# Performance work log

Measured on AMD Instinct MI355X. Metric: run time of the kernel, lower is better.

The kernel has to match this reference:

```python
import jax, jax.numpy as jnp
import numpy as np
from jax import lax

H = 145; W = 145; BANDS = 200; D_MODEL = 128; NUM_CLASSES = 17
# Mamba2 defaults: expand=2, headdim=64, d_state=128, d_conv=4, ngroups=1
D_INNER = 256; NHEADS = 4; HEADDIM = 64; D_STATE = 128; D_CONV = 4
D_IN_PROJ = 2 * D_INNER + 2 * D_STATE + NHEADS  # 772
CONV_DIM = D_INNER + 2 * D_STATE                # 512


def _gelu(x):
    return jax.nn.gelu(x, approximate=False)


def _ln(x, g, b, eps=1e-5):
    m = jnp.mean(x, -1, keepdims=True)
    v = jnp.mean((x - m) ** 2, -1, keepdims=True)
    return (x - m) * lax.rsqrt(v + eps) * g + b


def _adaptive_pool_last(x, out):
    # PyTorch AdaptiveAvgPool semantics along the last axis via integral image
    L = x.shape[-1]
    i = np.arange(out)
    starts = (i * L) // out
    ends = -((-(i + 1) * L) // out)  # ceil((i+1)*L/out)
    cs = jnp.concatenate([jnp.zeros(x.shape[:-1] + (1,), x.dtype), jnp.cumsum(x, -1)], -1)
    return (cs[..., ends] - cs[..., starts]) / jnp.asarray(ends - starts, x.dtype)


def _mamba2(u, in_w, conv_w, conv_b, dt_bias, A_log, D, norm_w, out_w):
    # u: (L, D_MODEL). Faithful Mamba2 reference path (batch=1 squeezed).
    L = u.shape[0]
    zxbcdt = u @ in_w                      # (L, 772)
    z = zxbcdt[:, :D_INNER]                # (L, 256)
    xBC = zxbcdt[:, D_INNER:2 * D_INNER + 2 * D_STATE]  # (L, 512)
    dt = jax.nn.softplus(zxbcdt[:, -NHEADS:] + dt_bias)  # (L, 4)
    # causal depthwise conv1d, kernel D_CONV, then SiLU
    xp = jnp.pad(xBC, ((D_CONV - 1, 0), (0, 0)))
    xBC = sum(xp[k:k + L] * conv_w[:, k] for k in range(D_CONV)) + conv_b
    xBC = jax.nn.silu(xBC)
    xh = xBC[:, :D_INNER].reshape(L, NHEADS, HEADDIM)     # (L, h, p)
    Bm = xBC[:, D_INNER:D_INNER + D_STATE]                # (L, n)
    Cm = xBC[:, D_INNER + D_STATE:]                       # (L, n)
    A = -jnp.exp(A_log)                                   # (h,)

    def step(state, inp):
        dt_t, x_t, B_t, C_t = inp          # (h,), (h,p), (n,), (n,)
        dA = jnp.exp(dt_t * A)             # (h,)
        state = state * dA[:, None, None] + (dt_t[:, None] * x_t)[:, :, None] * B_t[None, None, :]
        y_t = jnp.einsum('hpn,n->hp', state, C_t)
        return state, y_t

    s0 = jnp.zeros((NHEADS, HEADDIM, D_STATE), u.dtype)
    _, y = lax.scan(step, s0, (dt, xh, Bm, Cm))           # y: (L, h, p)
    y = y + D[None, :, None] * xh
    y = y.reshape(L, D_INNER) * jax.nn.silu(z)            # gated
    y = y * lax.rsqrt(jnp.mean(y * y, -1, keepdims=True) + 1e-5) * norm_w  # RMSNormGated
    return y @ out_w                                      # (L, D_MODEL)


def _forward(x, ln_pre_g, ln_pre_b, fe_w1, fe_b1, fe_w2, fe_b2,
             cv_w1, cv_b1, cv_w2, cv_b2, mp_w, mp_b, mp_ln_g, mp_ln_b,
             m_in_w, m_conv_w, m_conv_b, m_dt_bias, m_A_log, m_D, m_norm_w, m_out_w,
             cls_ln_g, cls_ln_b, cls_w1, cls_b1, cls_w2, cls_b2, cls_w3, cls_b3):
    h, w, _ = x.shape
    xn = _ln(x, ln_pre_g, ln_pre_b)
    # MLP feature branch
    f = _gelu(xn @ fe_w1 + fe_b1)
    f = _gelu(f @ fe_w2 + fe_b2)                          # (h, w, 128)
    # conv branch
    c = jnp.transpose(xn, (2, 0, 1))[None]                # (1, bands, h, w)
    dn = ('NCHW', 'OIHW', 'NCHW')
    c = lax.conv_general_dilated(c, cv_w1, (1, 1), [(2, 2), (2, 2)], dimension_numbers=dn)
    c = _gelu(c + cv_b1[None, :, None, None])             # (1, 32, 147, 147)
    c = lax.conv_general_dilated(c, cv_w2, (1, 1), [(1, 1), (1, 1)], dimension_numbers=dn)
    c = _gelu(c + cv_b2[None, :, None, None])             # (1, 64, 147, 147)
    c = _adaptive_pool_last(c, W)                         # pool width -> 145
    c = _adaptive_pool_last(c.swapaxes(-1, -2), H).swapaxes(-1, -2)  # pool height
    conv_feat = jnp.transpose(c[0], (1, 2, 0))            # (145, 145, 64)
    comb = jnp.concatenate([f, conv_feat], -1).reshape(h * w, 192)
    p = _gelu(_ln(comb @ mp_w + mp_b, mp_ln_g, mp_ln_b))  # (L, d_model)
    m = _mamba2(p, m_in_w, m_conv_w, m_conv_b, m_dt_bias, m_A_log, m_D, m_norm_w, m_out_w)
    r = m.reshape(h, w, D_MODEL)
    o = _ln(r, cls_ln_g, cls_ln_b)
    o = _gelu(o @ cls_w1 + cls_b1)
    o = _gelu(o @ cls_w2 + cls_b2)
    return o @ cls_w3 + cls_b3                            # (h, w, num_classes)


def setup_inputs() -> dict:
    key = jax.random.key(0)
    ks = jax.random.split(key, 16)
    def n(k, shape, s=0.02):
        return jax.random.normal(k, shape, jnp.float32) * s
    return dict(
        x=jax.random.normal(ks[0], (H, W, BANDS), jnp.float32),
        ln_pre_g=jnp.ones((BANDS,), jnp.float32), ln_pre_b=jnp.zeros((BANDS,), jnp.float32),
        fe_w1=n(ks[1], (BANDS, 256)), fe_b1=jnp.zeros((256,), jnp.float32),
        fe_w2=n(ks[2], (256, 128)), fe_b2=jnp.zeros((128,), jnp.float32),
        cv_w1=n(ks[3], (32, BANDS, 3, 3)), cv_b1=jnp.zeros((32,), jnp.float32),
        cv_w2=n(ks[4], (64, 32, 3, 3)), cv_b2=jnp.zeros((64,), jnp.float32),
        mp_w=n(ks[5], (192, D_MODEL)), mp_b=jnp.zeros((D_MODEL,), jnp.float32),
        mp_ln_g=jnp.ones((D_MODEL,), jnp.float32), mp_ln_b=jnp.zeros((D_MODEL,), jnp.float32),
        m_in_w=n(ks[6], (D_MODEL, D_IN_PROJ)),
        m_conv_w=n(ks[7], (CONV_DIM, D_CONV), 0.2), m_conv_b=jnp.zeros((CONV_DIM,), jnp.float32),
        m_dt_bias=jnp.full((NHEADS,), -4.0, jnp.float32),
        m_A_log=jnp.log(jnp.linspace(1.0, 16.0, NHEADS)).astype(jnp.float32),
        m_D=jnp.ones((NHEADS,), jnp.float32),
        m_norm_w=jnp.ones((D_INNER,), jnp.float32),
        m_out_w=n(ks[8], (D_INNER, D_MODEL)),
        cls_ln_g=jnp.ones((D_MODEL,), jnp.float32), cls_ln_b=jnp.zeros((D_MODEL,), jnp.float32),
        cls_w1=n(ks[9], (D_MODEL, 128)), cls_b1=jnp.zeros((128,), jnp.float32),
        cls_w2=n(ks[10], (128, 64)), cls_b2=jnp.zeros((64,), jnp.float32),
        cls_w3=n(ks[11], (64, NUM_CLASSES)), cls_b3=jnp.zeros((NUM_CLASSES,), jnp.float32),
    )


def reference(x, ln_pre_g, ln_pre_b, fe_w1, fe_b1, fe_w2, fe_b2,
              cv_w1, cv_b1, cv_w2, cv_b2, mp_w, mp_b, mp_ln_g, mp_ln_b,
              m_in_w, m_conv_w, m_conv_b, m_dt_bias, m_A_log, m_D, m_norm_w, m_out_w,
              cls_ln_g, cls_ln_b, cls_w1, cls_b1, cls_w2, cls_b2, cls_w3, cls_b3):
    return _forward(x, ln_pre_g, ln_pre_b, fe_w1, fe_b1, fe_w2, fe_b2,
                    cv_w1, cv_b1, cv_w2, cv_b2, mp_w, mp_b, mp_ln_g, mp_ln_b,
                    m_in_w, m_conv_w, m_conv_b, m_dt_bias, m_A_log, m_D, m_norm_w, m_out_w,
                    cls_ln_g, cls_ln_b, cls_w1, cls_b1, cls_w2, cls_b2, cls_w3, cls_b3)
```

## Files before the change

### kernel.cpp

```cpp
#include <hip/hip_runtime.h>
#include <math.h>

#define HW 21025
#define Hdim 145
#define Wdim 145
#define NBANDS 200
#define CONVH 147
#define CONVHW 21609
#define QC 64
#define NCH 329
#define DTP 21056
#define SP 72
#define SSD_GRID 1344

typedef __attribute__((ext_vector_type(4))) float fv4;
typedef __attribute__((ext_vector_type(8))) short short8;

#define OFF_XN   ((size_t)0)
#define OFF_F1   ((size_t)4205000)
#define OFF_COMB ((size_t)9587400)
#define OFF_P    ((size_t)13624200)
#define OFF_ZX   ((size_t)16315400)
#define OFF_XBC  ((size_t)32546700)
#define OFF_S    ((size_t)43311500)
// ... 3 lines not shown

__device__ __forceinline__ float gelu_f(float x){
    return 0.5f * x * (1.0f + erff(x * 0.70710678118654752440f));
}
__device__ __forceinline__ float silu_f(float x){
    return x / (1.0f + expf(-x));
}

__device__ __forceinline__ void bf16_split(float x, unsigned short& hs, unsigned short& ls){
    unsigned u = __float_as_uint(x);
    hs = (unsigned short)(u >> 16);
    float hif = __uint_as_float(u & 0xFFFF0000u);
    float lof = x - hif;
    ls = (unsigned short)(__float_as_uint(lof) >> 16);
}
__device__ __forceinline__ unsigned pack2(unsigned short a, unsigned short b){
    return (unsigned)a | ((unsigned)b << 16);
}
__device__ __forceinline__ unsigned packsplit(float x){
    unsigned short hs, ls;
    bf16_split(x, hs, ls);
    return ((unsigned)hs << 16) | (unsigned)ls;
}
__device__ __forceinline__ float unpackf(unsigned u){
    return __uint_as_float(u & 0xFFFF0000u) + __uint_as_float(u << 16);
}
__device__ __forceinline__ unsigned short bf16rnd(float x){
    unsigned u = __float_as_uint(x);
    unsigned r = u + 0x7FFFu + ((u >> 16) & 1u);
    return (unsigned short)(r >> 16);
}
__device__ __forceinline__ float bf16f(unsigned short h){
    return __uint_as_float((unsigned)h << 16);
}
__device__ __forceinline__ void unpack8(const unsigned* p, short8& h8, short8& l8){
    uint4 a = *reinterpret_cast<const uint4*>(p);
    uint4 b = *reinterpret_cast<const uint4*>(p + 4);
    unsigned v0 = a.x, v1 = a.y, v2 = a.z, v3 = a.w;
    unsigned v4 = b.x, v5 = b.y, v6 = b.z, v7 = b.w;
    h8[0]=(short)(v0>>16); l8[0]=(short)(v0&0xFFFFu);
    h8[1]=(short)(v1>>16); l8[1]=(short)(v1&0xFFFFu);
    h8[2]=(short)(v2>>16); l8[2]=(short)(v2&0xFFFFu);
    h8[3]=(short)(v3>>16); l8[3]=(short)(v3&0xFFFFu);
    h8[4]=(short)(v4>>16); l8[4]=(short)(v4&0xFFFFu);
    h8[5]=(short)(v5>>16); l8[5]=(short)(v5&0xFFFFu);
    h8[6]=(short)(v6>>16); l8[6]=(short)(v6&0xFFFFu);
    h8[7]=(short)(v7>>16); l8[7]=(short)(v7&0xFFFFu);
}

__device__ __forceinline__ bool gemm_decode(int bid, int NXB, int NYB, int& bx, int& by){
    int m = bid & 7;
    int r = bid >> 3;
    bx = r % NXB;
    by = (r / NXB) * 8 + m;
    return by < NYB;
}
__host__ __forceinline__ int gemm_grid(int NXB, int NYB){ return 8 * ((NYB + 7) / 8) * NXB; }

template<int ACT>
__global__ void ln_kernel(const float* __restrict__ in, const float* __restrict__ g,
                          const float* __restrict__ b, float* __restrict__ out, int D){
    int row = blockIdx.x, tid = threadIdx.x;
    const float* r = in + (size_t)row * D;
    float s = 0.f, s2 = 0.f;
    for (int i = tid; i < D; i += 256){ float v = r[i]; s += v; s2 += v*v; }
    __shared__ float r1[4], r2[4];
    #pragma unroll
    for (int o = 32; o > 0; o >>= 1){ s += __shfl_down(s, o); s2 += __shfl_down(s2, o); }
    if ((tid & 63) == 0){ r1[tid >> 6] = s; r2[tid >> 6] = s2; }
    __syncthreads();
    float S = r1[0] + r1[1] + r1[2] + r1[3];
    float S2 = r2[0] + r2[1] + r2[2] + r2[3];
    float mean = S / (float)D;
    float var = S2 / (float)D - mean * mean;
    float rs = rsqrtf(fmaxf(var, 0.f) + 1e-5f);
    float* o_ = out + (size_t)row * D;
    for (int i = tid; i < D; i += 256){
        float v = (r[i] - mean) * rs * g[i] + b[i];
        if (ACT == 1) v = gelu_f(v);
        o_[i] = v;
    }
}

template<int ACT, int MI>
__global__ __launch_bounds__(256) void gemm_mfma_w(const float* __restrict__ A, int lda,
                                                   const float* __restrict__ B, int ldb,
                                                   const float* __restrict__ bias,
                                                   const float* __restrict__ lng,
                                                   const float* __restrict__ lnb,
                                                   float* __restrict__ C, int ldc,
                                                   int M, int N, int K, int NXB, int NYB){
    const int SA = 40;
    const int BM = MI * 32;
    __shared__ __align__(16) unsigned short Ah[BM * SA], Al[BM * SA];
    __shared__ __align__(16) unsigned short Bh[128 * SA], Bl[128 * SA];
    __shared__ float rs1[2][BM], rs2_[2][BM];
    int bx, by;
    if (!gemm_decode(blockIdx.x, NXB, NYB, bx, by)) return;
    int tid = threadIdx.x;
    int lane = tid & 63, wid = tid >> 6;
    int wy = wid >> 1, wx = wid & 1;
    int bm = by * BM, bn = bx * 128;
    int l15 = lane & 15, g = lane >> 4;

    fv4 acc[MI][4];
    #pragma unroll
    for (int i = 0; i < MI; i++)
        #pragma unroll
        for (int j = 0; j < 4; j++) acc[i][j] = (fv4){0.f,0.f,0.f,0.f};

    int bcol = tid & 127;
    int bk16 = (tid >> 7) * 16;
    bool bcol_ok = (bn + bcol) < N;

    int nK = (K + 31) / 32;
    for (int ks = 0; ks < nK; ks++){
        int k0 = ks * 32;
        #pragma unroll
        for (int f = 0; f < MI; f++){
            int idx = tid * MI + f;
            int row = idx >> 3, qd = idx & 7;
            fv4 v = (fv4){0.f,0.f,0.f,0.f};
            if ((bm + row) < M && (k0 + qd * 4 + 4) <= K)
                v = *reinterpret_cast<const fv4*>(A + (size_t)(bm + row) * lda + k0 + qd * 4);
            unsigned short hs[4], ls[4];
            #pragma unroll
            for (int j = 0; j < 4; j++) bf16_split(v[j], hs[j], ls[j]);
            unsigned off = row * SA + qd * 4;
            *reinterpret_cast<uint2*>(&Ah[off]) = make_uint2(pack2(hs[0],hs[1]), pack2(hs[2],hs[3]));
            *reinterpret_cast<uint2*>(&Al[off]) = make_uint2(pack2(ls[0],ls[1]), pack2(ls[2],ls[3]));
        }
        {
            unsigned short hs[16], ls[16];
            #pragma unroll
            for (int j = 0; j < 16; j++){
                int kk = k0 + bk16 + j;
                float v = (bcol_ok && kk < K) ? B[(size_t)kk * ldb + bn + bcol] : 0.f;
                bf16_split(v, hs[j], ls[j]);
            }
            unsigned off = bcol * SA + bk16;
            *reinterpret_cast<uint4*>(&Bh[off]) = make_uint4(pack2(hs[0],hs[1]), pack2(hs[2],hs[3]),
                                                             pack2(hs[4],hs[5]), pack2(hs[6],hs[7]));
            *reinterpret_cast<uint4*>(&Bh[off + 8]) = make_uint4(pack2(hs[8],hs[9]), pack2(hs[10],hs[11]),
                                                                 pack2(hs[12],hs[13]), pack2(hs[14],hs[15]));
            *reinterpret_cast<uint4*>(&Bl[off]) = make_uint4(pack2(ls[0],ls[1]), pack2(ls[2],ls[3]),
                                                             pack2(ls[4],ls[5]), pack2(ls[6],ls[7]));
            *reinterpret_cast<uint4*>(&Bl[off + 8]) = make_uint4(pack2(ls[8],ls[9]), pack2(ls[10],ls[11]),
                                                                 pack2(ls[12],ls[13]), pack2(ls[14],ls[15]));
        }
        __syncthreads();
        short8 afh[MI], afl[MI], bfh[4], bfl[4];
        #pragma unroll
        for (int mi = 0; mi < MI; mi++){
            unsigned off = (wy * (MI * 16) + mi * 16 + l15) * SA + g * 8;
            afh[mi] = *reinterpret_cast<const short8*>(&Ah[off]);
            afl[mi] = *reinterpret_cast<const short8*>(&Al[off]);
        }
        #pragma unroll
        for (int ni = 0; ni < 4; ni++){
            unsigned off = (wx * 64 + ni * 16 + l15) * SA + g * 8;
            bfh[ni] = *reinterpret_cast<const short8*>(&Bh[off]);
            bfl[ni] = *reinterpret_cast<const short8*>(&Bl[off]);
        }
        #pragma unroll
        for (int mi = 0; mi < MI; mi++)
            #pragma unroll
            for (int ni = 0; ni < 4; ni++){
                acc[mi][ni] = __builtin_amdgcn_mfma_f32_16x16x32_bf16(afh[mi], bfh[ni], acc[mi][ni], 0, 0, 0);
                acc[mi][ni] = __builtin_amdgcn_mfma_f32_16x16x32_bf16(afh[mi], bfl[ni], acc[mi][ni], 0, 0, 0);
                acc[mi][ni] = __builtin_amdgcn_mfma_f32_16x16x32_bf16(afl[mi], bfh[ni], acc[mi][ni], 0, 0, 0);
            }
        __syncthreads();
    }
    float bv[4], lgv[4], lbv[4];
    #pragma unroll
    for (int ni = 0; ni < 4; ni++){
        int cc = bn + wx * 64 + ni * 16 + l15;
        bool ok = cc < N;
        bv[ni]  = (bias && ok) ? bias[cc] : 0.f;
        if (ACT >= 2){ lgv[ni] = ok ? lng[cc] : 1.f; lbv[ni] = ok ? lnb[cc] : 0.f; }
    }
    if (ACT >= 2){
        #pragma unroll
        for (int mi = 0; mi < MI; mi++)
            #pragma unroll
            for (int j = 0; j < 4; j++){
                float s = 0.f, s2 = 0.f;
                #pragma unroll
                for (int ni = 0; ni < 4; ni++){
                    float v = acc[mi][ni][j] + bv[ni];
                    s += v; s2 += v * v;
                }
                #pragma unroll
                for (int o = 1; o < 16; o <<= 1){
                    s += __shfl_xor(s, o); s2 += __shfl_xor(s2, o);
                }
                int row = wy * (MI * 16) + mi * 16 + g * 4 + j;
                if (l15 == 0){ rs1[wx][row] = s; rs2_[wx][row] = s2; }
            }
        __syncthreads();
        #pragma unroll
        for (int mi = 0; mi < MI; mi++)
            #pragma unroll
            for (int j = 0; j < 4; j++){
                int row = wy * (MI * 16) + mi * 16 + g * 4 + j;
                int rr = bm + row;
                if (rr >= M) continue;
                float S = rs1[0][row] + rs1[1][row];
                float S2 = rs2_[0][row] + rs2_[1][row];
                float mean = S / 128.f;
                float var = S2 / 128.f - mean * mean;
                float rsq = rsqrtf(fmaxf(var, 0.f) + 1e-5f);
                #pragma unroll
                for (int ni = 0; ni < 4; ni++){
                    int cc = bn + wx * 64 + ni * 16 + l15;
                    float v = acc[mi][ni][j] + bv[ni];
                    v = (v - mean) * rsq * lgv[ni] + lbv[ni];
                    if (ACT == 3) v = gelu_f(v);
                    C[(size_t)rr * ldc + cc] = v;
                }
            }
    } else {
        #pragma unroll
        for (int mi = 0; mi < MI; mi++)
            #pragma unroll
            for (int ni = 0; ni < 4; ni++){
                int cc = bn + wx * 64 + ni * 16 + l15;
                if (cc >= N) continue;
                #pragma unroll
                for (int j = 0; j < 4; j++){
                    int rr = bm + wy * (MI * 16) + mi * 16 + g * 4 + j;
                    if (rr >= M) continue;
                    float v = acc[mi][ni][j] + bv[ni];
                    if (ACT == 1) v = gelu_f(v);
                    C[(size_t)rr * ldc + cc] = v;
                }
            }
    }
}

template<int ACT>
__global__ __launch_bounds__(256) void gemm_mfma(const float* __restrict__ A, int lda,
                                                 const float* __restrict__ B,
                                                 const float* __restrict__ bias,
                                                 float* __restrict__ C, int ldc,
                                                 int M, int N, int K, int NXB, int NYB){
    const int SA = 40;
    __shared__ __align__(16) unsigned short Ah[128 * SA], Al[128 * SA];
    __shared__ __align__(16) unsigned short Bh[64 * SA],  Bl[64 * SA];
    int bx, by;
    if (!gemm_decode(blockIdx.x, NXB, NYB, bx, by)) return;
    int tid = threadIdx.x;
    int lane = tid & 63, wid = tid >> 6;
    int wy = wid >> 1, wx = wid & 1;
    int bm = by * 128, bn = bx * 64;
    int l15 = lane & 15, g = lane >> 4;

    fv4 acc[4][2];
    #pragma unroll
    for (int i = 0; i < 4; i++)
        #pragma unroll
        for (int j = 0; j < 2; j++) acc[i][j] = (fv4){0.f,0.f,0.f,0.f};

    int am = tid >> 1;
    int aq = (tid & 1) * 4;
    bool arow_ok = (bm + am) < M;
    int bn_t = tid & 63;
    int bk8 = (tid >> 6) * 8;
    bool bcol_ok = (bn + bn_t) < N;

    int nK = (K + 31) / 32;
    for (int ks = 0; ks < nK; ks++){
        int k0 = ks * 32;
        const float* Ap = A + (size_t)(bm + am) * lda + k0;
        #pragma unroll
        for (int f = 0; f < 4; f++){
            int kq = aq + f;
            fv4 v = (fv4){0.f,0.f,0.f,0.f};
            if (arow_ok && (k0 + kq * 4 + 4) <= K)
                v = *reinterpret_cast<const fv4*>(Ap + kq * 4);
            unsigned short hs[4], ls[4];
            #pragma unroll
            for (int j = 0; j < 4; j++) bf16_split(v[j], hs[j], ls[j]);
            unsigned off = am * SA + kq * 4;
            *reinterpret_cast<uint2*>(&Ah[off]) = make_uint2(pack2(hs[0],hs[1]), pack2(hs[2],hs[3]));
            *reinterpret_cast<uint2*>(&Al[off]) = make_uint2(pack2(ls[0],ls[1]), pack2(ls[2],ls[3]));
        }
        {
            unsigned short hs[8], ls[8];
            #pragma unroll
            for (int j = 0; j < 8; j++){
                int kk = k0 + bk8 + j;
                float v = (bcol_ok && kk < K) ? B[(size_t)kk * N + bn + bn_t] : 0.f;
                bf16_split(v, hs[j], ls[j]);
            }
            unsigned off = bn_t * SA + bk8;
            *reinterpret_cast<uint4*>(&Bh[off]) = make_uint4(pack2(hs[0],hs[1]), pack2(hs[2],hs[3]),
                                                             pack2(hs[4],hs[5]), pack2(hs[6],hs[7]));
            *reinterpret_cast<uint4*>(&Bl[off]) = make_uint4(pack2(ls[0],ls[1]), pack2(ls[2],ls[3]),
                                                             pack2(ls[4],ls[5]), pack2(ls[6],ls[7]));
        }
        __syncthreads();
        short8 afh[4], afl[4], bfh[2], bfl[2];
        #pragma unroll
        for (int mi = 0; mi < 4; mi++){
            unsigned off = (wy * 64 + mi * 16 + l15) * SA + g * 8;
            afh[mi] = *reinterpret_cast<const short8*>(&Ah[off]);
            afl[mi] = *reinterpret_cast<const short8*>(&Al[off]);
        }
        #pragma unroll
        for (int ni = 0; ni < 2; ni++){
            unsigned off = (wx * 32 + ni * 16 + l15) * SA + g * 8;
            bfh[ni] = *reinterpret_cast<const short8*>(&Bh[off]);
            bfl[ni] = *reinterpret_cast<const short8*>(&Bl[off]);
        }
        #pragma unroll
        for (int mi = 0; mi < 4; mi++)
            #pragma unroll
            for (int ni = 0; ni < 2; ni++){
                acc[mi][ni] = __builtin_amdgcn_mfma_f32_16x16x32_bf16(afh[mi], bfh[ni], acc[mi][ni], 0, 0, 0);
                acc[mi][ni] = __builtin_amdgcn_mfma_f32_16x16x32_bf16(afh[mi], bfl[ni], acc[mi][ni], 0, 0, 0);
                acc[mi][ni] = __builtin_amdgcn_mfma_f32_16x16x32_bf16(afl[mi], bfh[ni], acc[mi][ni], 0, 0, 0);
            }
        __syncthreads();
    }
    #pragma unroll
    for (int mi = 0; mi < 4; mi++){
        #pragma unroll
        for (int ni = 0; ni < 2; ni++){
            int cc = bn + wx * 32 + ni * 16 + l15;
            if (cc >= N) continue;
            float bv = bias ? bias[cc] : 0.f;
            #pragma unroll
            for (int j = 0; j < 4; j++){
                int rr = bm + wy * 64 + mi * 16 + g * 4 + j;
                if (rr >= M) continue;
                float v = acc[mi][ni][j] + bv;
                if (ACT == 1) v = gelu_f(v);
                C[(size_t)rr * ldc + cc] = v;
            }
        }
    }
}

__global__ __launch_bounds__(256) void dt_from_p(const float* __restrict__ p,
                                                 const float* __restrict__ w,
                                                 const float* __restrict__ dtb,
                                                 float* __restrict__ dtbT){
    __shared__ float wl[512];
    int tid = threadIdx.x;
    for (int i = tid; i < 512; i += 256){
        int k = i >> 2, h = i & 3;
        wl[i] = w[(size_t)k * 772 + 768 + h];
    }
    __syncthreads();
    int t = blockIdx.x * 64 + (tid >> 2);
    int h = tid & 3;
    if (t >= HW) return;
    const float* pr = p + (size_t)t * 128;
    float s = 0.f;
    for (int k = 0; k < 128; k += 4){
        fv4 v = *reinterpret_cast<const fv4*>(pr + k);
        s += v[0]*wl[k*4+h] + v[1]*wl[(k+1)*4+h] + v[2]*wl[(k+2)*4+h] + v[3]*wl[(k+3)*4+h];
    }
    s += dtb[h];
    dtbT[h * DTP + t] = (s > 20.f) ? s : log1pf(expf(s));
}

template<int IC, int OC, int NCHUNK>
__global__ void prep_w(const float* __restrict__ w, unsigned short* __restrict__ Wh,
                       unsigned short* __restrict__ Wl){
    const int KP = NCHUNK * 288;
    int idx = blockIdx.x * 256 + threadIdx.x;
    if (idx >= OC * KP) return;
    int o = idx / KP, k = idx % KP;
    int ch = k / 288, rest = k % 288, t = rest / 32, c = rest & 31;
    int ci = ch * 32 + c;
    float v = (ci < IC) ? w[((size_t)o * IC + ci) * 9 + t] : 0.f;
    unsigned short hs, ls;
    bf16_split(v, hs, ls);
    Wh[idx] = hs; Wl[idx] = ls;
}

template<int IC, int OC, int PAD, int NCHUNK, int NFRAG>
__global__ __launch_bounds__(256) void conv_mfma(const float* __restrict__ in,
                                                 int inH, int inW,
                                                 const unsigned short* __restrict__ Wh,
                                                 const unsigned short* __restrict__ Wl,
                                                 const float* __restrict__ bias,
                                                 float* __restrict__ out){
    const int KP = NCHUNK * 288;
    const int CST = 40;
    __shared__ __align__(16) unsigned short Xh[3 * 68 * CST], Xl[3 * 68 * CST];
    int y = blockIdx.y;
    int x0 = blockIdx.x * 64;
    int tid = threadIdx.x;
    int lane = tid & 63, wid = tid >> 6;
    int wy = wid >> 1, wx = wid & 1;
    int l15 = lane & 15, g = lane >> 4;

    fv4 acc[2][NFRAG];
    #pragma unroll
    for (int mi = 0; mi < 2; mi++)
        #pragma unroll
        for (int ni = 0; ni < NFRAG; ni++) acc[mi][ni] = (fv4){0.f,0.f,0.f,0.f};

    for (int ch = 0; ch < NCHUNK; ch++){
        int ci0 = ch * 32;
        if (ch > 0) __syncthreads();
        for (int e = tid; e < 3 * 68 * 8; e += 256){
            int qd = e & 7;
            int c  = (e >> 3) % 68;
            int r  = e / 544;
            int iy = y - PAD + r, ix = x0 - PAD + c;
            fv4 v = (fv4){0.f,0.f,0.f,0.f};
            if ((unsigned)iy < (unsigned)inH && (unsigned)ix < (unsigned)inW &&
                (ci0 + qd * 4 + 4) <= IC)
                v = *reinterpret_cast<const fv4*>(in + ((size_t)iy * inW + ix) * IC + ci0 + qd * 4);
            unsigned short hs[4], ls[4];
            #pragma unroll
            for (int j = 0; j < 4; j++) bf16_split(v[j], hs[j], ls[j]);
            unsigned off = (r * 68 + c) * CST + qd * 4;
            *reinterpret_cast<uint2*>(&Xh[off]) = make_uint2(pack2(hs[0],hs[1]), pack2(hs[2],hs[3]));
// ... 115 lines not shown
}

__global__ __launch_bounds__(256) void ssd_phaseA(const unsigned* __restrict__ xbcp,
                                                  const float* __restrict__ dtbT,
                                                  const float* __restrict__ A_log,
                                                  unsigned short* __restrict__ Sb,
                                                  float* __restrict__ chunkT){
    __shared__ __align__(16) unsigned short BTh[128 * SP], BTl[128 * SP];
    __shared__ __align__(16) unsigned short XTh[64 * SP],  XTl[64 * SP];
    __shared__ float cum[64], dth[64], wln[64];
    int c, h;
    if (!ssd_decode(blockIdx.x, c, h)) return;
    int t0 = c * QC, Q = min(QC, HW - t0);
    int tid = threadIdx.x;
    chunk_cumsum_t(dtbT, t0, Q, h, A_log, cum, dth);
    float T = cum[Q - 1];
    if (tid == 0) chunkT[c * 4 + h] = T;
    if (tid < 64) wln[tid] = (tid < Q) ? __expf(T - cum[tid]) * dth[tid] : 0.f;
    __syncthreads();
    for (int e2 = tid; e2 < 4096; e2 += 256){
        int nn = e2 & 127, sp = e2 >> 7;
        int s0 = 2 * sp;
        unsigned v0 = (s0 < Q)     ? xbcp[(size_t)(t0 + s0) * 512 + 256 + nn] : 0u;
        unsigned v1 = (s0 + 1 < Q) ? xbcp[(size_t)(t0 + s0 + 1) * 512 + 256 + nn] : 0u;
        *reinterpret_cast<unsigned*>(&BTh[nn * SP + s0]) = pack2((unsigned short)(v0 >> 16), (unsigned short)(v1 >> 16));
        *reinterpret_cast<unsigned*>(&BTl[nn * SP + s0]) = pack2((unsigned short)(v0 & 0xFFFFu), (unsigned short)(v1 & 0xFFFFu));
    }
    for (int e2 = tid; e2 < 2048; e2 += 256){
        int pp = e2 & 63, sp = e2 >> 6;
        int s0 = 2 * sp;
        float v0 = (s0 < Q)     ? unpackf(xbcp[(size_t)(t0 + s0) * 512 + h * 64 + pp]) * wln[s0] : 0.f;
        float v1 = (s0 + 1 < Q) ? unpackf(xbcp[(size_t)(t0 + s0 + 1) * 512 + h * 64 + pp]) * wln[s0 + 1] : 0.f;
        unsigned short h0, l0, h1, l1;
        bf16_split(v0, h0, l0); bf16_split(v1, h1, l1);
        *reinterpret_cast<unsigned*>(&XTh[pp * SP + s0]) = pack2(h0, h1);
        *reinterpret_cast<unsigned*>(&XTl[pp * SP + s0]) = pack2(l0, l1);
    }
    __syncthreads();
    int lane = tid & 63, wid = tid >> 6;
    int wy = wid >> 1, wx = wid & 1;
    int l15 = lane & 15, g = lane >> 4;
    fv4 acc[2][4];
    #pragma unroll
    for (int mi = 0; mi < 2; mi++)
        #pragma unroll
        for (int ni = 0; ni < 4; ni++) acc[mi][ni] = (fv4){0.f,0.f,0.f,0.f};
    #pragma unroll
    for (int ks = 0; ks < 2; ks++){
        short8 ah[2], al[2], bh_[4], bl_[4];
        #pragma unroll
        for (int mi = 0; mi < 2; mi++){
            unsigned off = (wy * 32 + mi * 16 + l15) * SP + ks * 32 + g * 8;
            ah[mi] = *reinterpret_cast<const short8*>(&XTh[off]);
            al[mi] = *reinterpret_cast<const short8*>(&XTl[off]);
        }
        #pragma unroll
        for (int ni = 0; ni < 4; ni++){
            unsigned off = (wx * 64 + ni * 16 + l15) * SP + ks * 32 + g * 8;
            bh_[ni] = *reinterpret_cast<const short8*>(&BTh[off]);
            bl_[ni] = *reinterpret_cast<const short8*>(&BTl[off]);
        }
        #pragma unroll
        for (int mi = 0; mi < 2; mi++)
            #pragma unroll
            for (int ni = 0; ni < 4; ni++){
                acc[mi][ni] = __builtin_amdgcn_mfma_f32_16x16x32_bf16(ah[mi], bh_[ni], acc[mi][ni], 0, 0, 0);
                acc[mi][ni] = __builtin_amdgcn_mfma_f32_16x16x32_bf16(ah[mi], bl_[ni], acc[mi][ni], 0, 0, 0);
                acc[mi][ni] = __builtin_amdgcn_mfma_f32_16x16x32_bf16(al[mi], bh_[ni], acc[mi][ni], 0, 0, 0);
            }
    }
    size_t sb = (size_t)(c * 4 + h) * 8192;
    #pragma unroll
    for (int mi = 0; mi < 2; mi++)
        #pragma unroll
        for (int ni = 0; ni < 4; ni++)
            #pragma unroll
            for (int j = 0; j < 4; j++){
                int p = wy * 32 + mi * 16 + g * 4 + j;
                int n = wx * 64 + ni * 16 + l15;
                Sb[sb + p * 128 + n] = bf16rnd(acc[mi][ni][j]);
            }
}

__global__ __launch_bounds__(256) void ssd_phaseB(unsigned short* __restrict__ Sb,
                                                  const float* __restrict__ chunkT){
    __shared__ float e[NCH];
    int tid = threadIdx.x;
    int idx = blockIdx.x * 256 + tid;
    int h = idx >> 13, pn = idx & 8191;
    for (int c = tid; c < NCH; c += 256) e[c] = __expf(chunkT[c * 4 + h]);
    __syncthreads();
    #define ADDR_(cc) Sb[((size_t)((cc) * 4 + h)) * 8192 + pn]
    unsigned short r0 = ADDR_(0), r1 = ADDR_(1), r2 = ADDR_(2), r3 = ADDR_(3);
    float s = 0.f;
    int c = 0;
    for (; c + 8 <= NCH; c += 4){
        unsigned short n0 = ADDR_(c + 4), n1 = ADDR_(c + 5), n2 = ADDR_(c + 6), n3 = ADDR_(c + 7);
        ADDR_(c) = bf16rnd(s);     s = fmaf(s, e[c],     bf16f(r0));
        ADDR_(c + 1) = bf16rnd(s); s = fmaf(s, e[c + 1], bf16f(r1));
        ADDR_(c + 2) = bf16rnd(s); s = fmaf(s, e[c + 2], bf16f(r2));
        ADDR_(c + 3) = bf16rnd(s); s = fmaf(s, e[c + 3], bf16f(r3));
        r0 = n0; r1 = n1; r2 = n2; r3 = n3;
    }
    for (; c < NCH; c++){
        unsigned short nx = (c + 4 < NCH) ? ADDR_(c + 4) : (unsigned short)0;
        float loc = bf16f(r0); r0 = r1; r1 = r2; r2 = r3; r3 = nx;
        ADDR_(c) = bf16rnd(s);
        s = fmaf(s, e[c], loc);
    }
    #undef ADDR_
}

__global__ __launch_bounds__(256) void ssd_phaseC(const unsigned* __restrict__ xbcp,
                                                  const float* __restrict__ zx,
                                                  const float* __restrict__ dtbT,
                                                  const float* __restrict__ A_log,
                                                  const float* __restrict__ Dvec,
                                                  const unsigned short* __restrict__ Sb,
                                                  float* __restrict__ y){
    __shared__ __align__(16) unsigned short U0[64 * SP];
    __shared__ __align__(16) unsigned short U1h[64 * SP], U1l[64 * SP];
    __shared__ float cum[64], dth[64];
    int c, h;
    if (!ssd_decode(blockIdx.x, c, h)) return;
    int t0 = c * QC, Q = min(QC, HW - t0);
    int tid = threadIdx.x;
    chunk_cumsum_t(dtbT, t0, Q, h, A_log, cum, dth);
    int lane = tid & 63, wid = tid >> 6;
    int wy = wid >> 1, wx = wid & 1;
    int l15 = lane & 15, g = lane >> 4;

    int trow[2], srow[2], prow[2];
    #pragma unroll
    for (int i = 0; i < 2; i++){
        trow[i] = min(t0 + wy * 32 + i * 16 + l15, HW - 1);
        srow[i] = min(t0 + wx * 32 + i * 16 + l15, HW - 1);
        prow[i] = wx * 32 + i * 16 + l15;
    }

    fv4 accG[2][2], accA[2][2];
    #pragma unroll
    for (int mi = 0; mi < 2; mi++)
        #pragma unroll
        for (int ni = 0; ni < 2; ni++){ accG[mi][ni] = (fv4){0.f,0.f,0.f,0.f}; accA[mi][ni] = (fv4){0.f,0.f,0.f,0.f}; }

    const unsigned short* Sbase = Sb + (size_t)(c * 4 + h) * 8192;
    #pragma unroll
    for (int k0 = 0; k0 < 128; k0 += 32){
        short8 ah[2], al[2], bh[2], bl[2], sh[2];
        #pragma unroll
        for (int mi = 0; mi < 2; mi++)
            unpack8(xbcp + (size_t)trow[mi] * 512 + 384 + k0 + g * 8, ah[mi], al[mi]);
        #pragma unroll
        for (int ni = 0; ni < 2; ni++){
            unpack8(xbcp + (size_t)srow[ni] * 512 + 256 + k0 + g * 8, bh[ni], bl[ni]);
            sh[ni] = *reinterpret_cast<const short8*>(Sbase + prow[ni] * 128 + k0 + g * 8);
        }
        #pragma unroll
        for (int mi = 0; mi < 2; mi++)
            #pragma unroll
            for (int ni = 0; ni < 2; ni++){
                accG[mi][ni] = __builtin_amdgcn_mfma_f32_16x16x32_bf16(ah[mi], bh[ni], accG[mi][ni], 0, 0, 0);
                accG[mi][ni] = __builtin_amdgcn_mfma_f32_16x16x32_bf16(ah[mi], bl[ni], accG[mi][ni], 0, 0, 0);
                accG[mi][ni] = __builtin_amdgcn_mfma_f32_16x16x32_bf16(al[mi], bh[ni], accG[mi][ni], 0, 0, 0);
                accA[mi][ni] = __builtin_amdgcn_mfma_f32_16x16x32_bf16(ah[mi], sh[ni], accA[mi][ni], 0, 0, 0);
                accA[mi][ni] = __builtin_amdgcn_mfma_f32_16x16x32_bf16(al[mi], sh[ni], accA[mi][ni], 0, 0, 0);
            }
    }
    #pragma unroll
    for (int mi = 0; mi < 2; mi++)
        #pragma unroll
        for (int ni = 0; ni < 2; ni++)
            #pragma unroll
            for (int j = 0; j < 4; j++){
                int t = wy * 32 + mi * 16 + g * 4 + j;
                int s = wx * 32 + ni * 16 + l15;
                float pv = 0.f;
                if (s <= t && s < Q)
                    pv = accG[mi][ni][j] * __expf(cum[t] - cum[s]) * dth[s];
                U0[t * SP + s] = bf16rnd(pv);
            }
    for (int e2 = tid; e2 < 2048; e2 += 256){
        int pp = e2 & 63, sp = e2 >> 6;
        int s0 = 2 * sp;
        unsigned v0 = (s0 < Q)     ? xbcp[(size_t)(t0 + s0) * 512 + h * 64 + pp] : 0u;
        unsigned v1 = (s0 + 1 < Q) ? xbcp[(size_t)(t0 + s0 + 1) * 512 + h * 64 + pp] : 0u;
        *reinterpret_cast<unsigned*>(&U1h[pp * SP + s0]) = pack2((unsigned short)(v0 >> 16), (unsigned short)(v1 >> 16));
        *reinterpret_cast<unsigned*>(&U1l[pp * SP + s0]) = pack2((unsigned short)(v0 & 0xFFFFu), (unsigned short)(v1 & 0xFFFFu));
    }
    __syncthreads();
    fv4 accY[2][2];
    #pragma unroll
    for (int mi = 0; mi < 2; mi++)
        #pragma unroll
        for (int ni = 0; ni < 2; ni++)
            #pragma unroll
            for (int j = 0; j < 4; j++){
                int t = wy * 32 + mi * 16 + g * 4 + j;
                accY[mi][ni][j] = __expf(cum[t]) * accA[mi][ni][j];
            }
    #pragma unroll
    for (int kk = 0; kk < 2; kk++){
        short8 ph[2], xh[2], xl[2];
        #pragma unroll
        for (int mi = 0; mi < 2; mi++){
            unsigned off = (wy * 32 + mi * 16 + l15) * SP + kk * 32 + g * 8;
            ph[mi] = *reinterpret_cast<const short8*>(&U0[off]);
        }
        #pragma unroll
        for (int ni = 0; ni < 2; ni++){
            unsigned off = (wx * 32 + ni * 16 + l15) * SP + kk * 32 + g * 8;
            xh[ni] = *reinterpret_cast<const short8*>(&U1h[off]);
            xl[ni] = *reinterpret_cast<const short8*>(&U1l[off]);
        }
        #pragma unroll
        for (int mi = 0; mi < 2; mi++)
            #pragma unroll
            for (int ni = 0; ni < 2; ni++){
                accY[mi][ni] = __builtin_amdgcn_mfma_f32_16x16x32_bf16(ph[mi], xh[ni], accY[mi][ni], 0, 0, 0);
                accY[mi][ni] = __builtin_amdgcn_mfma_f32_16x16x32_bf16(ph[mi], xl[ni], accY[mi][ni], 0, 0, 0);
            }
    }
    float Dh = Dvec[h];
    #pragma unroll
    for (int mi = 0; mi < 2; mi++)
        #pragma unroll
        for (int ni = 0; ni < 2; ni++)
            #pragma unroll
            for (int j = 0; j < 4; j++){
                int t = wy * 32 + mi * 16 + g * 4 + j;
                if (t >= Q) continue;
                int p = wx * 32 + ni * 16 + l15;
                float xv = unpackf(xbcp[(size_t)(t0 + t) * 512 + h * 64 + p]);
                float zv = zx[(size_t)(t0 + t) * 772 + h * 64 + p];
                y[(size_t)(t0 + t) * 256 + h * 64 + p] = (accY[mi][ni][j] + Dh * xv) * silu_f(zv);
            }
}

__global__ void rms_kernel(float* __restrict__ y, const float* __restrict__ nw){
    int row = blockIdx.x, tid = threadIdx.x;
    float v = y[(size_t)row * 256 + tid];
    float s = v * v;
    __shared__ float r1[4];
    #pragma unroll
    for (int o = 32; o > 0; o >>= 1) s += __shfl_down(s, o);
    if ((tid & 63) == 0) r1[tid >> 6] = s;
    __syncthreads();
    float S = r1[0] + r1[1] + r1[2] + r1[3];
    float rs = rsqrtf(S / 256.f + 1e-5f);
    y[(size_t)row * 256 + tid] = v * rs * nw[tid];
}

extern "C" void kernel_launch(void* const* d_in, const int* in_sizes, int n_in,
                              void* d_out, int out_size, void* d_ws, size_t ws_size,
                              hipStream_t stream){
    (void)in_sizes; (void)n_in; (void)out_size; (void)ws_size;
    const float* x        = (const float*)d_in[0];
    const float* ln_pre_g = (const float*)d_in[1];
    const float* ln_pre_b = (const float*)d_in[2];
    const float* fe_w1    = (const float*)d_in[3];
    const float* fe_b1    = (const float*)d_in[4];
    const float* fe_w2    = (const float*)d_in[5];
    const float* fe_b2    = (const float*)d_in[6];
    const float* cv_w1    = (const float*)d_in[7];
    const float* cv_b1    = (const float*)d_in[8];
    const float* cv_w2    = (const float*)d_in[9];
    const float* cv_b2    = (const float*)d_in[10];
    const float* mp_w     = (const float*)d_in[11];
    const float* mp_b     = (const float*)d_in[12];
    const float* mp_ln_g  = (const float*)d_in[13];
    const float* mp_ln_b  = (const float*)d_in[14];
    const float* m_in_w   = (const float*)d_in[15];
    const float* m_conv_w = (const float*)d_in[16];
    const float* m_conv_b = (const float*)d_in[17];
    const float* m_dtb    = (const float*)d_in[18];
    const float* m_A_log  = (const float*)d_in[19];
    const float* m_D      = (const float*)d_in[20];
    const float* m_norm_w = (const float*)d_in[21];
    const float* m_out_w  = (const float*)d_in[22];
    const float* cls_ln_g = (const float*)d_in[23];
    const float* cls_ln_b = (const float*)d_in[24];
    const float* cls_w1   = (const float*)d_in[25];
    const float* cls_b1   = (const float*)d_in[26];
    const float* cls_w2   = (const float*)d_in[27];
    const float* cls_b2   = (const float*)d_in[28];
    const float* cls_w3   = (const float*)d_in[29];
    const float* cls_b3   = (const float*)d_in[30];

    float* ws   = (float*)d_ws;
    float* xn   = ws + OFF_XN;
    float* f1   = ws + OFF_F1;
    float* comb = ws + OFF_COMB;
    float* p    = ws + OFF_P;
    float* zx   = ws + OFF_ZX;
    unsigned* xbcp = (unsigned*)(ws + OFF_XBC);
    unsigned short* Sb = (unsigned short*)(ws + OFF_S);
    float* dtbT = ws + OFF_DT;
    float* chkT = ws + OFF_CT;
    float* c1h  = ws + OFF_XBC;
    float* c2h  = ws + OFF_XBC + 691488;
    float* ybuf = ws + OFF_F1;
    float* cls0 = ws + OFF_XN;
    float* cls1 = ws + OFF_P;
    float* cls2 = ws + OFF_COMB + 2691200;
    unsigned short* W1h = (unsigned short*)(ws + OFF_W);
    unsigned short* W1l = (unsigned short*)(ws + OFF_W + 32256);
    unsigned short* W2h = (unsigned short*)(ws + OFF_W + 64512);
    unsigned short* W2l = (unsigned short*)(ws + OFF_W + 73728);

    prep_w<200, 32, 7><<<(32 * 2016 + 255) / 256, 256, 0, stream>>>(cv_w1, W1h, W1l);
    prep_w<32, 64, 1><<<(64 * 288 + 255) / 256, 256, 0, stream>>>(cv_w2, W2h, W2l);
    ln_kernel<0><<<HW, 256, 0, stream>>>(x, ln_pre_g, ln_pre_b, xn, NBANDS);
    gemm_mfma_w<1, 4><<<gemm_grid(2, 165), 256, 0, stream>>>(xn, 200, fe_w1, 256, fe_b1,
        (const float*)nullptr, (const float*)nullptr, f1, 256, HW, 256, 200, 2, 165);
    gemm_mfma_w<1, 2><<<gemm_grid(1, 329), 256, 0, stream>>>(f1, 256, fe_w2, 128, fe_b2,
        (const float*)nullptr, (const float*)nullptr, comb, 192, HW, 128, 256, 1, 329);
    conv_mfma<200, 32, 2, 7, 1><<<dim3(3, CONVH), 256, 0, stream>>>(xn, Hdim, Wdim, W1h, W1l, cv_b1, c1h);
    conv_mfma<32, 64, 1, 1, 2><<<dim3(3, CONVH), 256, 0, stream>>>(c1h, CONVH, CONVH, W2h, W2l, cv_b2, c2h);
    pool_kernel<<<(HW * 64 + 255) / 256, 256, 0, stream>>>(c2h, comb);
    gemm_mfma_w<3, 2><<<gemm_grid(1, 329), 256, 0, stream>>>(comb, 192, mp_w, 128, mp_b,
        mp_ln_g, mp_ln_b, p, 128, HW, 128, 192, 1, 329);
    gemm_mfma_w<0, 4><<<gemm_grid(6, 165), 256, 0, stream>>>(p, 128, m_in_w, 772,
        (const float*)nullptr, (const float*)nullptr, (const float*)nullptr,
        zx, 772, HW, 768, 128, 6, 165);
    dt_from_p<<<(HW + 63) / 64, 256, 0, stream>>>(p, m_in_w, m_dtb, dtbT);
    conv1d_tiled<<<dim3(4, NCH), 256, 0, stream>>>(zx, m_conv_w, m_conv_b, xbcp);
    ssd_phaseA<<<SSD_GRID, 256, 0, stream>>>(xbcp, dtbT, m_A_log, Sb, chkT);
    ssd_phaseB<<<128, 256, 0, stream>>>(Sb, chkT);
    ssd_phaseC<<<SSD_GRID, 256, 0, stream>>>(xbcp, zx, dtbT, m_A_log, m_D, Sb, ybuf);
    rms_kernel<<<HW, 256, 0, stream>>>(ybuf, m_norm_w);
    gemm_mfma_w<2, 2><<<gemm_grid(1, 329), 256, 0, stream>>>(ybuf, 256, m_out_w, 128,
        (const float*)nullptr, cls_ln_g, cls_ln_b, cls0, 128, HW, 128, 256, 1, 329);
    gemm_mfma_w<1, 2><<<gemm_grid(1, 329), 256, 0, stream>>>(cls0, 128, cls_w1, 128, cls_b1,
        (const float*)nullptr, (const float*)nullptr, cls1, 128, HW, 128, 128, 1, 329);
    gemm_mfma<1><<<gemm_grid(1, 165), 256, 0, stream>>>(cls1, 128, cls_w2, cls_b2, cls2, 64, HW, 64, 128, 1, 165);
    gemm_mfma<0><<<gemm_grid(1, 165), 256, 0, stream>>>(cls2, 64, cls_w3, cls_b3, (float*)d_out, 17, HW, 17, 64, 1, 165);
}
```

Before: 469.3 us.

## Fuse RMSNorm into out-proj GEMM, fuse classifier tail, retune SSD phaseB

Removes the standalone RMSNorm kernel. Its per-row RMS is now computed in the out-projection GEMM prologue and applied to the A tile, while the norm weight is folded into the B tile. The last two classifier GEMMs are fused into one kernel that keeps the GELU intermediate in shared memory and removes an HBM round-trip. SSD phaseB moves from 128 blocks of 256 threads to 512 blocks of 64 threads for more parallelism. The prologue re-reads each A row, and the tail kernel has a 17-column output with padding waste.

```diff
diff --git a/kernel.cpp b/kernel.cpp
--- a/kernel.cpp
+++ b/kernel.cpp
@@ -109,12 +109,13 @@
     }
 }
 
-template<int ACT, int MI>
+template<int ACT, int MI, int ARMS>
 __global__ __launch_bounds__(256) void gemm_mfma_w(const float* __restrict__ A, int lda,
                                                    const float* __restrict__ B, int ldb,
                                                    const float* __restrict__ bias,
                                                    const float* __restrict__ lng,
                                                    const float* __restrict__ lnb,
+                                                   const float* __restrict__ arms_w,
                                                    float* __restrict__ C, int ldc,
                                                    int M, int N, int K, int NXB, int NYB){
     const int SA = 40;
@@ -122,6 +123,8 @@
     __shared__ __align__(16) unsigned short Ah[BM * SA], Al[BM * SA];
     __shared__ __align__(16) unsigned short Bh[128 * SA], Bl[128 * SA];
     __shared__ float rs1[2][BM], rs2_[2][BM];
+    __shared__ float ascale[BM];
+    __shared__ float wn[256];
     int bx, by;
     if (!gemm_decode(blockIdx.x, NXB, NYB, bx, by)) return;
     int tid = threadIdx.x;
@@ -130,6 +133,23 @@
     int bm = by * BM, bn = bx * 128;
     int l15 = lane & 15, g = lane >> 4;
 
+    if (ARMS){
+        for (int i = tid; i < K && i < 256; i += 256) wn[i] = arms_w[i];
+        int row = tid >> 2, seg = tid & 3;
+        float ss = 0.f;
+        if (row < BM && (bm + row) < M){
+            const float* ar = A + (size_t)(bm + row) * lda + seg * (K >> 2);
+            for (int k = 0; k < (K >> 2); k += 4){
+                fv4 v = *reinterpret_cast<const fv4*>(ar + k);
+                ss += v[0]*v[0] + v[1]*v[1] + v[2]*v[2] + v[3]*v[3];
+            }
+        }
+        ss += __shfl_xor(ss, 1);
+        ss += __shfl_xor(ss, 2);
+        if ((tid & 3) == 0 && row < BM) ascale[row] = rsqrtf(ss / (float)K + 1e-5f);
+        __syncthreads();
+    }
+
     fv4 acc[MI][4];
     #pragma unroll
     for (int i = 0; i < MI; i++)
@@ -150,6 +170,7 @@
             fv4 v = (fv4){0.f,0.f,0.f,0.f};
             if ((bm + row) < M && (k0 + qd * 4 + 4) <= K)
                 v = *reinterpret_cast<const fv4*>(A + (size_t)(bm + row) * lda + k0 + qd * 4);
+            if (ARMS) v *= ascale[row];
             unsigned short hs[4], ls[4];
             #pragma unroll
             for (int j = 0; j < 4; j++) bf16_split(v[j], hs[j], ls[j]);
@@ -163,6 +184,7 @@
             for (int j = 0; j < 16; j++){
                 int kk = k0 + bk16 + j;
                 float v = (bcol_ok && kk < K) ? B[(size_t)kk * ldb + bn + bcol] : 0.f;
+                if (ARMS && kk < K) v *= wn[kk];
                 bf16_split(v, hs[j], ls[j]);
             }
             unsigned off = bcol * SA + bk16;
@@ -266,50 +288,57 @@
     }
 }
 
-template<int ACT>
-__global__ __launch_bounds__(256) void gemm_mfma(const float* __restrict__ A, int lda,
-                                                 const float* __restrict__ B,
-                                                 const float* __restrict__ bias,
-                                                 float* __restrict__ C, int ldc,
-                                                 int M, int N, int K, int NXB, int NYB){
+__global__ __launch_bounds__(256) void cls_tail(const float* __restrict__ A,
+                                                const float* __restrict__ W2,
+                                                const float* __restrict__ b2,
+                                                const float* __restrict__ W3,
+                                                const float* __restrict__ b3,
+                                                float* __restrict__ out,
+                                                int M, int NYB){
     const int SA = 40;
-    __shared__ __align__(16) unsigned short Ah[128 * SA], Al[128 * SA];
-    __shared__ __align__(16) unsigned short Bh[64 * SA],  Bl[64 * SA];
+    __shared__ __align__(16) unsigned short Ah[64 * SA], Al[64 * SA];
+    __shared__ __align__(16) unsigned short Bh[64 * SA], Bl[64 * SA];
+    __shared__ __align__(16) unsigned short A2h[64 * 72], A2l[64 * 72];
+    __shared__ __align__(16) unsigned short B3h[32 * 72], B3l[32 * 72];
     int bx, by;
-    if (!gemm_decode(blockIdx.x, NXB, NYB, bx, by)) return;
+    if (!gemm_decode(blockIdx.x, 1, NYB, bx, by)) return;
     int tid = threadIdx.x;
     int lane = tid & 63, wid = tid >> 6;
     int wy = wid >> 1, wx = wid & 1;
-    int bm = by * 128, bn = bx * 64;
+    int bm = by * 64;
     int l15 = lane & 15, g = lane >> 4;
 
-    fv4 acc[4][2];
-    #pragma unroll
-    for (int i = 0; i < 4; i++)
-        #pragma unroll
-        for (int j = 0; j < 2; j++) acc[i][j] = (fv4){0.f,0.f,0.f,0.f};
-
-    int am = tid >> 1;
-    int aq = (tid & 1) * 4;
-    bool arow_ok = (bm + am) < M;
+    for (int e = tid; e < 2048; e += 256){
+        int n = e >> 6, k = e & 63;
+        float v = (n < 17) ? W3[(size_t)k * 17 + n] : 0.f;
+        unsigned short hs, ls;
+        bf16_split(v, hs, ls);
+        B3h[n * 72 + k] = hs;
+        B3l[n * 72 + k] = ls;
+    }
+
+    fv4 acc[2][2];
+    #pragma unroll
+    for (int mi = 0; mi < 2; mi++)
+        #pragma unroll
+        for (int ni = 0; ni < 2; ni++) acc[mi][ni] = (fv4){0.f,0.f,0.f,0.f};
+
     int bn_t = tid & 63;
     int bk8 = (tid >> 6) * 8;
-    bool bcol_ok = (bn + bn_t) < N;
-
-    int nK = (K + 31) / 32;
-    for (int ks = 0; ks < nK; ks++){
+    #pragma unroll
+    for (int ks = 0; ks < 4; ks++){
         int k0 = ks * 32;
-        const float* Ap = A + (size_t)(bm + am) * lda + k0;
-        #pragma unroll
-        for (int f = 0; f < 4; f++){
-            int kq = aq + f;
+        #pragma unroll
+        for (int f = 0; f < 2; f++){
+            int idx = tid * 2 + f;
+            int row = idx >> 3, qd = idx & 7;
             fv4 v = (fv4){0.f,0.f,0.f,0.f};
-            if (arow_ok && (k0 + kq * 4 + 4) <= K)
-                v = *reinterpret_cast<const fv4*>(Ap + kq * 4);
+            if ((bm + row) < M)
+                v = *reinterpret_cast<const fv4*>(A + (size_t)(bm + row) * 128 + k0 + qd * 4);
             unsigned short hs[4], ls[4];
             #pragma unroll
             for (int j = 0; j < 4; j++) bf16_split(v[j], hs[j], ls[j]);
-            unsigned off = am * SA + kq * 4;
+            unsigned off = row * SA + qd * 4;
             *reinterpret_cast<uint2*>(&Ah[off]) = make_uint2(pack2(hs[0],hs[1]), pack2(hs[2],hs[3]));
             *reinterpret_cast<uint2*>(&Al[off]) = make_uint2(pack2(ls[0],ls[1]), pack2(ls[2],ls[3]));
         }
@@ -318,7 +347,7 @@
             #pragma unroll
             for (int j = 0; j < 8; j++){
                 int kk = k0 + bk8 + j;
-                float v = (bcol_ok && kk < K) ? B[(size_t)kk * N + bn + bn_t] : 0.f;
+                float v = W2[(size_t)kk * 64 + bn_t];
                 bf16_split(v, hs[j], ls[j]);
             }
             unsigned off = bn_t * SA + bk8;
@@ -328,10 +357,10 @@
                                                              pack2(ls[4],ls[5]), pack2(ls[6],ls[7]));
         }
         __syncthreads();
-        short8 afh[4], afl[4], bfh[2], bfl[2];
-        #pragma unroll
-        for (int mi = 0; mi < 4; mi++){
-            unsigned off = (wy * 64 + mi * 16 + l15) * SA + g * 8;
+        short8 afh[2], afl[2], bfh[2], bfl[2];
+        #pragma unroll
+        for (int mi = 0; mi < 2; mi++){
+            unsigned off = (wy * 32 + mi * 16 + l15) * SA + g * 8;
             afh[mi] = *reinterpret_cast<const short8*>(&Ah[off]);
             afl[mi] = *reinterpret_cast<const short8*>(&Al[off]);
         }
@@ -342,7 +371,7 @@
             bfl[ni] = *reinterpret_cast<const short8*>(&Bl[off]);
         }
         #pragma unroll
-        for (int mi = 0; mi < 4; mi++)
+        for (int mi = 0; mi < 2; mi++)
             #pragma unroll
             for (int ni = 0; ni < 2; ni++){
                 acc[mi][ni] = __builtin_amdgcn_mfma_f32_16x16x32_bf16(afh[mi], bfh[ni], acc[mi][ni], 0, 0, 0);
@@ -352,20 +381,50 @@
         __syncthreads();
     }
     #pragma unroll
-    for (int mi = 0; mi < 4; mi++){
+    for (int mi = 0; mi < 2; mi++)
         #pragma unroll
         for (int ni = 0; ni < 2; ni++){
-            int cc = bn + wx * 32 + ni * 16 + l15;
-            if (cc >= N) continue;
-            float bv = bias ? bias[cc] : 0.f;
+            int col = wx * 32 + ni * 16 + l15;
+            float bv = b2[col];
             #pragma unroll
             for (int j = 0; j < 4; j++){
-                int rr = bm + wy * 64 + mi * 16 + g * 4 + j;
-                if (rr >= M) continue;
-                float v = acc[mi][ni][j] + bv;
-                if (ACT == 1) v = gelu_f(v);
-                C[(size_t)rr * ldc + cc] = v;
-            }
+                int row = wy * 32 + mi * 16 + g * 4 + j;
+                float v = gelu_f(acc[mi][ni][j] + bv);
+                unsigned short hs, ls;
+                bf16_split(v, hs, ls);
+                A2h[row * 72 + col] = hs;
+                A2l[row * 72 + col] = ls;
+            }
+        }
+    __syncthreads();
+    fv4 acc3[2];
+    acc3[0] = (fv4){0.f,0.f,0.f,0.f};
+    acc3[1] = (fv4){0.f,0.f,0.f,0.f};
+    #pragma unroll
+    for (int ks = 0; ks < 2; ks++){
+        unsigned aoff = (wid * 16 + l15) * 72 + ks * 32 + g * 8;
+        short8 a2h = *reinterpret_cast<const short8*>(&A2h[aoff]);
+        short8 a2l = *reinterpret_cast<const short8*>(&A2l[aoff]);
+        #pragma unroll
+        for (int ni = 0; ni < 2; ni++){
+            unsigned boff = (ni * 16 + l15) * 72 + ks * 32 + g * 8;
+            short8 b3h_ = *reinterpret_cast<const short8*>(&B3h[boff]);
+            short8 b3l_ = *reinterpret_cast<const short8*>(&B3l[boff]);
+            acc3[ni] = __builtin_amdgcn_mfma_f32_16x16x32_bf16(a2h, b3h_, acc3[ni], 0, 0, 0);
+            acc3[ni] = __builtin_amdgcn_mfma_f32_16x16x32_bf16(a2h, b3l_, acc3[ni], 0, 0, 0);
+            acc3[ni] = __builtin_amdgcn_mfma_f32_16x16x32_bf16(a2l, b3h_, acc3[ni], 0, 0, 0);
+        }
+    }
+    #pragma unroll
+    for (int ni = 0; ni < 2; ni++){
+        int col = ni * 16 + l15;
+        if (col >= 17) continue;
+        float bv = b3[col];
+        #pragma unroll
+        for (int j = 0; j < 4; j++){
+            int row = bm + wid * 16 + g * 4 + j;
+            if (row >= M) continue;
+            out[(size_t)row * 17 + col] = acc3[ni][j] + bv;
         }
     }
 }
@@ -647,13 +706,13 @@
             }
 }
 
-__global__ __launch_bounds__(256) void ssd_phaseB(unsigned short* __restrict__ Sb,
-                                                  const float* __restrict__ chunkT){
+__global__ __launch_bounds__(64) void ssd_phaseB(unsigned short* __restrict__ Sb,
+                                                 const float* __restrict__ chunkT){
     __shared__ float e[NCH];
     int tid = threadIdx.x;
-    int idx = blockIdx.x * 256 + tid;
+    int idx = blockIdx.x * 64 + tid;
     int h = idx >> 13, pn = idx & 8191;
-    for (int c = tid; c < NCH; c += 256) e[c] = __expf(chunkT[c * 4 + h]);
+    for (int c = tid; c < NCH; c += 64) e[c] = __expf(chunkT[c * 4 + h]);
     __syncthreads();
     #define ADDR_(cc) Sb[((size_t)((cc) * 4 + h)) * 8192 + pn]
     unsigned short r0 = ADDR_(0), r1 = ADDR_(1), r2 = ADDR_(2), r3 = ADDR_(3);
@@ -800,20 +859,6 @@
                 float zv = zx[(size_t)(t0 + t) * 772 + h * 64 + p];
                 y[(size_t)(t0 + t) * 256 + h * 64 + p] = (accY[mi][ni][j] + Dh * xv) * silu_f(zv);
             }
-}
-
-__global__ void rms_kernel(float* __restrict__ y, const float* __restrict__ nw){
-    int row = blockIdx.x, tid = threadIdx.x;
-    float v = y[(size_t)row * 256 + tid];
-    float s = v * v;
-    __shared__ float r1[4];
-    #pragma unroll
-    for (int o = 32; o > 0; o >>= 1) s += __shfl_down(s, o);
-    if ((tid & 63) == 0) r1[tid >> 6] = s;
-    __syncthreads();
-    float S = r1[0] + r1[1] + r1[2] + r1[3];
-    float rs = rsqrtf(S / 256.f + 1e-5f);
-    y[(size_t)row * 256 + tid] = v * rs * nw[tid];
 }
 
 extern "C" void kernel_launch(void* const* d_in, const int* in_sizes, int n_in,
@@ -867,37 +912,35 @@
     float* ybuf = ws + OFF_F1;
     float* cls0 = ws + OFF_XN;
     float* cls1 = ws + OFF_P;
-    float* cls2 = ws + OFF_COMB + 2691200;
     unsigned short* W1h = (unsigned short*)(ws + OFF_W);
     unsigned short* W1l = (unsigned short*)(ws + OFF_W + 32256);
     unsigned short* W2h = (unsigned short*)(ws + OFF_W + 64512);
     unsigned short* W2l = (unsigned short*)(ws + OFF_W + 73728);
+    const float* NUL = (const float*)nullptr;
 
     prep_w<200, 32, 7><<<(32 * 2016 + 255) / 256, 256, 0, stream>>>(cv_w1, W1h, W1l);
     prep_w<32, 64, 1><<<(64 * 288 + 255) / 256, 256, 0, stream>>>(cv_w2, W2h, W2l);
     ln_kernel<0><<<HW, 256, 0, stream>>>(x, ln_pre_g, ln_pre_b, xn, NBANDS);
-    gemm_mfma_w<1, 4><<<gemm_grid(2, 165), 256, 0, stream>>>(xn, 200, fe_w1, 256, fe_b1,
-        (const float*)nullptr, (const float*)nullptr, f1, 256, HW, 256, 200, 2, 165);
-    gemm_mfma_w<1, 2><<<gemm_grid(1, 329), 256, 0, stream>>>(f1, 256, fe_w2, 128, fe_b2,
-        (const float*)nullptr, (const float*)nullptr, comb, 192, HW, 128, 256, 1, 329);
+    gemm_mfma_w<1, 4, 0><<<gemm_grid(2, 165), 256, 0, stream>>>(xn, 200, fe_w1, 256, fe_b1,
+        NUL, NUL, NUL, f1, 256, HW, 256, 200, 2, 165);
+    gemm_mfma_w<1, 2, 0><<<gemm_grid(1, 329), 256, 0, stream>>>(f1, 256, fe_w2, 128, fe_b2,
+        NUL, NUL, NUL, comb, 192, HW, 128, 256, 1, 329);
     conv_mfma<200, 32, 2, 7, 1><<<dim3(3, CONVH), 256, 0, stream>>>(xn, Hdim, Wdim, W1h, W1l, cv_b1, c1h);
     conv_mfma<32, 64, 1, 1, 2><<<dim3(3, CONVH), 256, 0, stream>>>(c1h, CONVH, CONVH, W2h, W2l, cv_b2, c2h);
     pool_kernel<<<(HW * 64 + 255) / 256, 256, 0, stream>>>(c2h, comb);
-    gemm_mfma_w<3, 2><<<gemm_grid(1, 329), 256, 0, stream>>>(comb, 192, mp_w, 128, mp_b,
-        mp_ln_g, mp_ln_b, p, 128, HW, 128, 192, 1, 329);
-    gemm_mfma_w<0, 4><<<gemm_grid(6, 165), 256, 0, stream>>>(p, 128, m_in_w, 772,
-        (const float*)nullptr, (const float*)nullptr, (const float*)nullptr,
-        zx, 772, HW, 768, 128, 6, 165);
+    gemm_mfma_w<3, 2, 0><<<gemm_grid(1, 329), 256, 0, stream>>>(comb, 192, mp_w, 128, mp_b,
+        mp_ln_g, mp_ln_b, NUL, p, 128, HW, 128, 192, 1, 329);
+    gemm_mfma_w<0, 4, 0><<<gemm_grid(6, 165), 256, 0, stream>>>(p, 128, m_in_w, 772,
+        NUL, NUL, NUL, NUL, zx, 772, HW, 768, 128, 6, 165);
     dt_from_p<<<(HW + 63) / 64, 256, 0, stream>>>(p, m_in_w, m_dtb, dtbT);
     conv1d_tiled<<<dim3(4, NCH), 256, 0, stream>>>(zx, m_conv_w, m_conv_b, xbcp);
     ssd_phaseA<<<SSD_GRID, 256, 0, stream>>>(xbcp, dtbT, m_A_log, Sb, chkT);
-    ssd_phaseB<<<128, 256, 0, stream>>>(Sb, chkT);
+    ssd_phaseB<<<512, 64, 0, stream>>>(Sb, chkT);
     ssd_phaseC<<<SSD_GRID, 256, 0, stream>>>(xbcp, zx, dtbT, m_A_log, m_D, Sb, ybuf);
-    rms_kernel<<<HW, 256, 0, stream>>>(ybuf, m_norm_w);
-    gemm_mfma_w<2, 2><<<gemm_grid(1, 329), 256, 0, stream>>>(ybuf, 256, m_out_w, 128,
-        (const float*)nullptr, cls_ln_g, cls_ln_b, cls0, 128, HW, 128, 256, 1, 329);
-    gemm_mfma_w<1, 2><<<gemm_grid(1, 329), 256, 0, stream>>>(cls0, 128, cls_w1, 128, cls_b1,
-        (const float*)nullptr, (const float*)nullptr, cls1, 128, HW, 128, 128, 1, 329);
-    gemm_mfma<1><<<gemm_grid(1, 165), 256, 0, stream>>>(cls1, 128, cls_w2, cls_b2, cls2, 64, HW, 64, 128, 1, 165);
-    gemm_mfma<0><<<gemm_grid(1, 165), 256, 0, stream>>>(cls2, 64, cls_w3, cls_b3, (float*)d_out, 17, HW, 17, 64, 1, 165);
-}
+    gemm_mfma_w<2, 2, 1><<<gemm_grid(1, 329), 256, 0, stream>>>(ybuf, 256, m_out_w, 128,
+        NUL, cls_ln_g, cls_ln_b, m_norm_w, cls0, 128, HW, 128, 256, 1, 329);
+    gemm_mfma_w<1, 2, 0><<<gemm_grid(1, 329), 256, 0, stream>>>(cls0, 128, cls_w1, 128, cls_b1,
+        NUL, NUL, NUL, cls1, 128, HW, 128, 128, 1, 329);
+    cls_tail<<<gemm_grid(1, 329), 256, 0, stream>>>(cls1, cls_w2, cls_b2, cls_w3, cls_b3,
+        (float*)d_out, HW, 329);
+}
```

Measured after the change: 475.0 us. Within noise of the previous version (+1.2%).
